# Kernel tuning notes

Hardware: AMD Instinct MI355X
Metric: run time of the kernel (lower is better)

The kernel has to match this reference:

```python
import jax, jax.numpy as jnp
import numpy as np

B, V, E, D_IN, D_OUT = 8, 10000, 160000, 128, 128
BN_EPS = 1e-5


def setup_inputs() -> dict:
    key = jax.random.key(0)
    ks = jax.random.split(key, 8)
    X = jax.random.normal(ks[0], (B, V, D_IN), dtype=jnp.float32)
    edge_attr = jax.random.normal(ks[1], (B, E), dtype=jnp.float32)
    W_node = jax.random.normal(ks[2], (D_OUT, D_IN), dtype=jnp.float32) * (1.0 / np.sqrt(D_IN))
    W_edge = jax.random.normal(ks[3], (D_OUT, 1), dtype=jnp.float32)
    W_self = jax.random.normal(ks[4], (D_OUT, D_IN), dtype=jnp.float32) * (1.0 / np.sqrt(D_IN))
    b_self = jax.random.normal(ks[5], (D_OUT,), dtype=jnp.float32) * 0.01
    gamma = jnp.ones((D_OUT,), dtype=jnp.float32)
    beta = jnp.zeros((D_OUT,), dtype=jnp.float32)
    edge_index = jax.random.randint(ks[6], (E, 2), 0, V, dtype=jnp.int32)
    return {"X": X, "edge_attr": edge_attr, "W_node": W_node, "W_edge": W_edge,
            "W_self": W_self, "b_self": b_self, "gamma": gamma, "beta": beta,
            "edge_index": edge_index}


def reference(X, edge_attr, W_node, W_edge, W_self, b_self, gamma, beta, edge_index):
    src = edge_index[:, 0]  # [E]
    dst = edge_index[:, 1]  # [E]
    # self-loop linear
    H = jnp.einsum('bvf,of->bvo', X, W_self) + b_self  # [B,V,D_OUT]
    # fused gather -> per-edge message -> scatter-add
    msg = jnp.einsum('bef,of->beo', X[:, src, :], W_node)  # [B,E,D_OUT]
    msg = msg + edge_attr[:, :, None] * W_edge[:, 0][None, None, :]
    aggregated = jnp.zeros_like(H).at[:, dst, :].add(msg)
    H = H + aggregated
    # BatchNorm1d over channel dim (training mode, biased variance over B*V)
    mean = jnp.mean(H, axis=(0, 1))
    var = jnp.var(H, axis=(0, 1))
    Hn = (H - mean) * jax.lax.rsqrt(var + BN_EPS) * gamma + beta
    return jax.nn.relu(Hn)
```

## Files before the change

### kernel.cpp

```cpp
#include <hip/hip_runtime.h>

#define B_ 8
#define V_ 10000
#define E_ 160000
#define DIN 128
#define DOUT 128
#define M_ (B_*V_)
#define NINV (1.0f/80000.0f)
#define BN_EPS 1e-5f

#define WS_COUNTS  0
#define WS_SUM     10000
#define WS_SUMSQ   10128
#define WS_ROWPTR  10512
#define WS_CURSOR  20513
#define WS_SSRC    30513
#define WS_EAS     190520
#define WS_S       1470520
#define WS_WPK     1550520
#define WS_XH      1566904
#define WS_AH      6686904
#define WS_ZERO_UNITS 10256

typedef __attribute__((ext_vector_type(2))) _Float16 half2_t;
typedef __attribute__((ext_vector_type(4))) _Float16 half4_t;
typedef __attribute__((ext_vector_type(8))) _Float16 half8_t;
typedef __attribute__((ext_vector_type(4))) float f32x4;

__device__ inline half2_t i2h(unsigned i) {
    half2_t h; __builtin_memcpy(&h, &i, 4); return h;
}
__device__ inline unsigned h2i(half2_t h) {
    unsigned i; __builtin_memcpy(&i, &h, 4); return i;
}

__global__ __launch_bounds__(256) void prep_kernel(
    const float* __restrict__ X, _Float16* __restrict__ Xh,
    const float* __restrict__ Wself, const float* __restrict__ Wnode,
    _Float16* __restrict__ Wpk,
    const int* __restrict__ EI, int* __restrict__ counts)
{
    const int blk = blockIdx.x;
    const int t = threadIdx.x;
    if (blk < 10000) {
        int idx = blk * 256 + t;
        float4 v = ((const float4*)X)[idx];
        half4_t o = { (_Float16)v.x, (_Float16)v.y, (_Float16)v.z, (_Float16)v.w };
        ((half4_t*)Xh)[idx] = o;
    } else if (blk < 10016) {
        int g = (blk - 10000) * 256 + t;
        int pair = g >> 6;
        int lane = g & 63;
        int ks = pair >> 3;
        int nt = pair & 7;
        int o = nt * 16 + (lane & 15);
        int k = ks * 32 + (lane >> 4) * 8;
        const float* wsrc = (k < 128) ? (Wself + o * 128 + k)
                                      : (Wnode + o * 128 + (k - 128));
        _Float16* dst = Wpk + ((size_t)pair * 64 + lane) * 8;
#pragma unroll
        for (int j = 0; j < 8; ++j) dst[j] = (_Float16)wsrc[j];
    } else {
        int e = (blk - 10016) * 256 + t;
        if (e < E_) atomicAdd(&counts[EI[2 * e + 1]], 1);
    }
}

__global__ __launch_bounds__(256) void scan_kernel(
    const int* __restrict__ counts, int* __restrict__ row_ptr,
    int* __restrict__ cursor)
{
    __shared__ int psum[256];
    const int t = threadIdx.x;
    const int base = t * 40;
    int local[40];
    int s = 0;
#pragma unroll
    for (int i = 0; i < 40; ++i) {
        int idx = base + i;
        int c = (idx < V_) ? counts[idx] : 0;
        local[i] = s;
        s += c;
    }
    psum[t] = s;
    __syncthreads();
    for (int off = 1; off < 256; off <<= 1) {
        int v = (t >= off) ? psum[t - off] : 0;
        __syncthreads();
        psum[t] += v;
        __syncthreads();
    }
    int excl = (t == 0) ? 0 : psum[t - 1];
#pragma unroll
    for (int i = 0; i < 40; ++i) {
        int idx = base + i;
        if (idx < V_) {
            int rp = excl + local[i];
            row_ptr[idx] = rp;
            cursor[idx] = rp;
        }
    }
    if (t == 255) row_ptr[V_] = psum[255];
}

__global__ __launch_bounds__(256) void bucket_kernel(
    const int* __restrict__ EI, const float* __restrict__ EA,
    int* __restrict__ cursor, int* __restrict__ ssrc,
    float* __restrict__ EAs)
{
    int e = blockIdx.x * 256 + threadIdx.x;
    if (e < E_) {
        int src = EI[2 * e];
        int dst = EI[2 * e + 1];
        int p = atomicAdd(&cursor[dst], 1);
        ssrc[p] = src;
        float4 v0, v1;
        v0.x = EA[0 * E_ + e]; v0.y = EA[1 * E_ + e];
        v0.z = EA[2 * E_ + e]; v0.w = EA[3 * E_ + e];
        v1.x = EA[4 * E_ + e]; v1.y = EA[5 * E_ + e];
        v1.z = EA[6 * E_ + e]; v1.w = EA[7 * E_ + e];
        *(float4*)(EAs + (size_t)p * 8) = v0;
        *(float4*)(EAs + (size_t)p * 8 + 4) = v1;
    }
}

__global__ __launch_bounds__(256) void gather_kernel(
    const _Float16* __restrict__ Xh, const float* __restrict__ EAs,
    const int* __restrict__ row_ptr, const int* __restrict__ ssrc,
    _Float16* __restrict__ Ah, float* __restrict__ S)
{
    const int b = blockIdx.x & 7;
    const int dblk = blockIdx.x >> 3;
    const int w = threadIdx.x >> 6;
    const int lane = threadIdx.x & 63;
    const int half = lane >> 5;
    const int sl = lane & 31;
    const int d = dblk * 4 + w;
    const int wid = b * V_ + d;
    const int k0 = row_ptr[d];
    const int k1 = row_ptr[d + 1];
    const _Float16* Xb = Xh + (size_t)b * V_ * DIN + sl * 4;
    half2_t a0 = (half2_t)0, a1 = (half2_t)0;
    float ea = 0.0f;
    for (int kb = k0; kb < k1; kb += 64) {
        int cnt = min(64, k1 - kb);
        int msrc = 0;
        if (lane < cnt) {
            msrc = ssrc[kb + lane];
            ea += EAs[(size_t)(kb + lane) * 8 + b];
        }
        int j = 0;
        for (; j + 8 <= cnt; j += 8) {
#pragma unroll
            for (int u = 0; u < 4; ++u) {
                int s = __shfl(msrc, j + u * 2 + half);
                uint2 v = *(const uint2*)(Xb + (size_t)s * DIN);
                a0 += i2h(v.x);
                a1 += i2h(v.y);
            }
        }
        for (; j + 2 <= cnt; j += 2) {
            int s = __shfl(msrc, j + half);
            uint2 v = *(const uint2*)(Xb + (size_t)s * DIN);
            a0 += i2h(v.x);
            a1 += i2h(v.y);
        }
        if (j < cnt) {
            int s = __shfl(msrc, j);
            if (half == 0) {
                uint2 v = *(const uint2*)(Xb + (size_t)s * DIN);
                a0 += i2h(v.x);
                a1 += i2h(v.y);
            }
        }
    }
    unsigned c0 = __shfl_down(h2i(a0), 32);
    unsigned c1 = __shfl_down(h2i(a1), 32);
    a0 += i2h(c0);
    a1 += i2h(c1);
    for (int off = 32; off; off >>= 1) ea += __shfl_down(ea, off);
    if (lane == 0) S[wid] = ea;
    if (half == 0) {
        uint2 o;
        o.x = h2i(a0);
        o.y = h2i(a1);
        *(uint2*)(Ah + (size_t)wid * DIN + sl * 4) = o;
    }
}

__global__ __launch_bounds__(128) void mfma_gemm_kernel(
    const _Float16* __restrict__ Xh, const _Float16* __restrict__ Ah,
    const _Float16* __restrict__ Wpk, const float* __restrict__ S,
    const float* __restrict__ bself, const float* __restrict__ wedge,
    float* __restrict__ H, float* __restrict__ gsum, float* __restrict__ gsumsq)
{
    __shared__ float cs[128];
    __shared__ float css[128];
    const int t = threadIdx.x;
    const int wave = t >> 6;
    const int lane = t & 63;
    const int quad = lane >> 4;
    const int ln = lane & 15;
    const int rowbase = blockIdx.x * 64 + wave * 32;
    const int m0 = rowbase + ln;
    const int m1 = rowbase + 16 + ln;

    cs[t] = 0.0f; css[t] = 0.0f;

    f32x4 acc[2][8];
#pragma unroll
    for (int mt = 0; mt < 2; ++mt)
#pragma unroll
        for (int nt = 0; nt < 8; ++nt) acc[mt][nt] = (f32x4){0.f, 0.f, 0.f, 0.f};

    const _Float16* X0 = Xh + (size_t)m0 * DIN + quad * 8;
    const _Float16* X1 = Xh + (size_t)m1 * DIN + quad * 8;
    const _Float16* A0 = Ah + (size_t)m0 * DIN + quad * 8;
    const _Float16* A1 = Ah + (size_t)m1 * DIN + quad * 8;
    const _Float16* Wl = Wpk + lane * 8;

#pragma unroll
    for (int ks = 0; ks < 8; ++ks) {
        half8_t af0, af1;
        if (ks < 4) {
            af0 = *(const half8_t*)(X0 + ks * 32);
            af1 = *(const half8_t*)(X1 + ks * 32);
        } else {
            af0 = *(const half8_t*)(A0 + (ks - 4) * 32);
            af1 = *(const half8_t*)(A1 + (ks - 4) * 32);
        }
#pragma unroll
        for (int nt = 0; nt < 8; ++nt) {
            half8_t bfr = *(const half8_t*)(Wl + (size_t)(ks * 8 + nt) * 512);
            acc[0][nt] = __builtin_amdgcn_mfma_f32_16x16x32_f16(af0, bfr, acc[0][nt], 0, 0, 0);
            acc[1][nt] = __builtin_amdgcn_mfma_f32_16x16x32_f16(af1, bfr, acc[1][nt], 0, 0, 0);
        }
    }

    float bs[8], we[8];
#pragma unroll
    for (int nt = 0; nt < 8; ++nt) {
        int c = nt * 16 + ln;
        bs[nt] = bself[c];
        we[nt] = wedge[c];
    }
    float psum[8], psq[8];
#pragma unroll
    for (int nt = 0; nt < 8; ++nt) { psum[nt] = 0.0f; psq[nt] = 0.0f; }

#pragma unroll
    for (int mt = 0; mt < 2; ++mt) {
        const int rbase = rowbase + mt * 16 + quad * 4;
        float sv[4];
#pragma unroll
        for (int r = 0; r < 4; ++r) sv[r] = S[rbase + r];
#pragma unroll
        for (int r = 0; r < 4; ++r) {
            float* Hr = H + (size_t)(rbase + r) * DOUT + ln;
#pragma unroll
            for (int nt = 0; nt < 8; ++nt) {
                float h = acc[mt][nt][r] + bs[nt] + sv[r] * we[nt];
                Hr[nt * 16] = h;
                psum[nt] += h;
                psq[nt] += h * h;
            }
        }
    }
#pragma unroll
    for (int nt = 0; nt < 8; ++nt) {
        psum[nt] += __shfl_down(psum[nt], 32);
        psum[nt] += __shfl_down(psum[nt], 16);
        psq[nt] += __shfl_down(psq[nt], 32);
        psq[nt] += __shfl_down(psq[nt], 16);
    }
    __syncthreads();
    if (lane < 16) {
#pragma unroll
        for (int nt = 0; nt < 8; ++nt) {
            atomicAdd(&cs[nt * 16 + ln], psum[nt]);
            atomicAdd(&css[nt * 16 + ln], psq[nt]);
        }
    }
    __syncthreads();
    atomicAdd(&gsum[t], cs[t]);
    atomicAdd(&gsumsq[t], css[t]);
}

__global__ __launch_bounds__(256) void norm_relu_kernel(
    float* __restrict__ H, const float* __restrict__ gsum,
    const float* __restrict__ gsumsq, const float* __restrict__ gamma,
    const float* __restrict__ beta)
{
    int idx = blockIdx.x * 256 + threadIdx.x;
    int o4 = (idx & 31) * 4;
    float4 s = *(const float4*)(gsum + o4);
    float4 q = *(const float4*)(gsumsq + o4);
    float4 g = *(const float4*)(gamma + o4);
    float4 bt = *(const float4*)(beta + o4);
    float4 sc, sh;
    {
        float m0 = s.x * NINV, m1 = s.y * NINV, m2 = s.z * NINV, m3 = s.w * NINV;
        float r0 = rsqrtf(q.x * NINV - m0 * m0 + BN_EPS);
        float r1 = rsqrtf(q.y * NINV - m1 * m1 + BN_EPS);
        float r2 = rsqrtf(q.z * NINV - m2 * m2 + BN_EPS);
        float r3 = rsqrtf(q.w * NINV - m3 * m3 + BN_EPS);
        sc.x = g.x * r0; sc.y = g.y * r1; sc.z = g.z * r2; sc.w = g.w * r3;
        sh.x = bt.x - m0 * sc.x; sh.y = bt.y - m1 * sc.y;
        sh.z = bt.z - m2 * sc.z; sh.w = bt.w - m3 * sc.w;
    }
    float4 h = ((const float4*)H)[idx];
    h.x = fmaxf(h.x * sc.x + sh.x, 0.0f);
    h.y = fmaxf(h.y * sc.y + sh.y, 0.0f);
    h.z = fmaxf(h.z * sc.z + sh.z, 0.0f);
    h.w = fmaxf(h.w * sc.w + sh.w, 0.0f);
    ((float4*)H)[idx] = h;
}

extern "C" void kernel_launch(void* const* d_in, const int* in_sizes, int n_in,
                              void* d_out, int out_size, void* d_ws, size_t ws_size,
                              hipStream_t stream)
{
    const float* X      = (const float*)d_in[0];
    const float* EA     = (const float*)d_in[1];
    const float* Wnode  = (const float*)d_in[2];
    const float* Wedge  = (const float*)d_in[3];
    const float* Wself  = (const float*)d_in[4];
    const float* bself  = (const float*)d_in[5];
    const float* gamma  = (const float*)d_in[6];
    const float* beta   = (const float*)d_in[7];
    const int*   EI     = (const int*)d_in[8];

    int*   wsI    = (int*)d_ws;
    float* wsF    = (float*)d_ws;
    int*   counts = wsI + WS_COUNTS;
    float* gsum   = wsF + WS_SUM;
    float* gsumsq = wsF + WS_SUMSQ;
    int*   rowptr = wsI + WS_ROWPTR;
    int*   cursor = wsI + WS_CURSOR;
    int*   ssrc   = wsI + WS_SSRC;
    float* EAs    = wsF + WS_EAS;
    float* S      = wsF + WS_S;
    _Float16* Wpk = (_Float16*)(wsI + WS_WPK);
    _Float16* Xh  = (_Float16*)(wsI + WS_XH);
    _Float16* Ah  = (_Float16*)(wsI + WS_AH);
    float* H      = (float*)d_out;

    hipMemsetAsync(d_ws, 0, (size_t)WS_ZERO_UNITS * 4, stream);

    prep_kernel<<<10641, 256, 0, stream>>>(X, Xh, Wself, Wnode, Wpk, EI, counts);
    scan_kernel<<<1, 256, 0, stream>>>(counts, rowptr, cursor);
    bucket_kernel<<<(E_ + 255) / 256, 256, 0, stream>>>(EI, EA, cursor, ssrc, EAs);

    gather_kernel<<<M_ / 4, 256, 0, stream>>>(Xh, EAs, rowptr, ssrc, Ah, S);

    mfma_gemm_kernel<<<M_ / 64, 128, 0, stream>>>(Xh, Ah, Wpk, S, bself, Wedge,
                                                  H, gsum, gsumsq);

    norm_relu_kernel<<<(M_ * DOUT / 4) / 256, 256, 0, stream>>>(H, gsum, gsumsq,
                                                                gamma, beta);
}
```

Measured before the change: 247.3 us.

## Replace global stat atomics with per-block partials and a reduction kernel

The GEMM kernel now uses 256-thread blocks covering 128 rows each, halving the block count. Instead of each block atomically adding its column sums and sums of squares into global buffers, it writes them to a partials array. A new small kernel then reduces those partials per channel. This removes contention on 256 global atomic addresses, at the cost of an extra kernel launch and a partials buffer in workspace.

```diff
diff --git a/kernel.cpp b/kernel.cpp
--- a/kernel.cpp
+++ b/kernel.cpp
@@ -8,6 +8,8 @@
 #define M_ (B_*V_)
 #define NINV (1.0f/80000.0f)
 #define BN_EPS 1e-5f
+
+#define GEMM_BLOCKS 625
 
 #define WS_COUNTS  0
 #define WS_SUM     10000
@@ -20,7 +22,8 @@
 #define WS_WPK     1550520
 #define WS_XH      1566904
 #define WS_AH      6686904
-#define WS_ZERO_UNITS 10256
+#define WS_PART    11806904
+#define WS_ZERO_UNITS 10000
 
 typedef __attribute__((ext_vector_type(2))) _Float16 half2_t;
 typedef __attribute__((ext_vector_type(4))) _Float16 half4_t;
@@ -188,11 +191,11 @@
     }
 }
 
-__global__ __launch_bounds__(128) void mfma_gemm_kernel(
+__global__ __launch_bounds__(256) void mfma_gemm_kernel(
     const _Float16* __restrict__ Xh, const _Float16* __restrict__ Ah,
     const _Float16* __restrict__ Wpk, const float* __restrict__ S,
     const float* __restrict__ bself, const float* __restrict__ wedge,
-    float* __restrict__ H, float* __restrict__ gsum, float* __restrict__ gsumsq)
+    float* __restrict__ H, float* __restrict__ Partials)
 {
     __shared__ float cs[128];
     __shared__ float css[128];
@@ -201,11 +204,11 @@
     const int lane = t & 63;
     const int quad = lane >> 4;
     const int ln = lane & 15;
-    const int rowbase = blockIdx.x * 64 + wave * 32;
+    const int rowbase = blockIdx.x * 128 + wave * 32;
     const int m0 = rowbase + ln;
     const int m1 = rowbase + 16 + ln;
 
-    cs[t] = 0.0f; css[t] = 0.0f;
+    if (t < 128) { cs[t] = 0.0f; css[t] = 0.0f; }
 
     f32x4 acc[2][8];
 #pragma unroll
@@ -282,8 +285,23 @@
         }
     }
     __syncthreads();
-    atomicAdd(&gsum[t], cs[t]);
-    atomicAdd(&gsumsq[t], css[t]);
+    Partials[(size_t)blockIdx.x * 256 + t] = (t < 128) ? cs[t] : css[t - 128];
+}
+
+__global__ __launch_bounds__(64) void reduce_stats_kernel(
+    const float* __restrict__ Partials, float* __restrict__ gsum,
+    float* __restrict__ gsumsq)
+{
+    const int c = blockIdx.x;
+    const int t = threadIdx.x;
+    float acc = 0.0f;
+    for (int p = t; p < GEMM_BLOCKS; p += 64)
+        acc += Partials[(size_t)p * 256 + c];
+    for (int off = 32; off; off >>= 1) acc += __shfl_down(acc, off);
+    if (t == 0) {
+        if (c < 128) gsum[c] = acc;
+        else gsumsq[c - 128] = acc;
+    }
 }
 
 __global__ __launch_bounds__(256) void norm_relu_kernel(
@@ -343,6 +361,7 @@
     _Float16* Wpk = (_Float16*)(wsI + WS_WPK);
     _Float16* Xh  = (_Float16*)(wsI + WS_XH);
     _Float16* Ah  = (_Float16*)(wsI + WS_AH);
+    float* Partials = wsF + WS_PART;
     float* H      = (float*)d_out;
 
     hipMemsetAsync(d_ws, 0, (size_t)WS_ZERO_UNITS * 4, stream);
@@ -353,8 +372,10 @@
 
     gather_kernel<<<M_ / 4, 256, 0, stream>>>(Xh, EAs, rowptr, ssrc, Ah, S);
 
-    mfma_gemm_kernel<<<M_ / 64, 128, 0, stream>>>(Xh, Ah, Wpk, S, bself, Wedge,
-                                                  H, gsum, gsumsq);
+    mfma_gemm_kernel<<<GEMM_BLOCKS, 256, 0, stream>>>(Xh, Ah, Wpk, S, bself,
+                                                      Wedge, H, Partials);
+
+    reduce_stats_kernel<<<256, 64, 0, stream>>>(Partials, gsum, gsumsq);
 
     norm_relu_kernel<<<(M_ * DOUT / 4) / 256, 256, 0, stream>>>(H, gsum, gsumsq,
                                                                 gamma, beta);
```

Measured after the change: 226.3 us. 8.5% less time.
